# Kernel optimization log

Measured on AMD Instinct MI355X. Metric: run time of the kernel, lower is better.

## Reference

```python
import jax, jax.numpy as jnp
import numpy as np

N, E, IN, ED, H, HID, OUT, G = 50000, 800000, 128, 16, 4, 64, 128, 64
NEG_SLOPE = 0.2


def _glorot(key, shape):
    fan_in, fan_out = shape[0], shape[-1]
    lim = float(np.sqrt(6.0 / (fan_in + fan_out)))
    return jax.random.uniform(key, shape, jnp.float32, -lim, lim)


def setup_inputs() -> dict:
    key = jax.random.key(0)
    ks = jax.random.split(key, 32)
    inp = {}
    inp['x'] = jax.random.normal(ks[0], (N, IN), jnp.float32)
    inp['edge_index'] = jax.random.randint(ks[1], (2, E), 0, N)
    inp['edge_attr'] = jax.random.normal(ks[2], (E, ED), jnp.float32)
    inp['batch'] = jnp.sort(jax.random.randint(ks[3], (N,), 0, G))
    # layer dims: (in_channels, out_channels_per_head, concat)
    dims = [(IN, HID, True), (H * HID, HID, True), (H * HID, OUT, False)]
    k = 4
    for i, (cin, c, concat) in enumerate(dims):
        inp[f'W{i}'] = _glorot(ks[k], (cin, H * c)); k += 1
        inp[f'asrc{i}'] = _glorot(ks[k], (1, H, c)); k += 1
        inp[f'adst{i}'] = _glorot(ks[k], (1, H, c)); k += 1
        inp[f'We{i}'] = _glorot(ks[k], (ED, H * c)); k += 1
        inp[f'ae{i}'] = _glorot(ks[k], (1, H, c)); k += 1
        inp[f'b{i}'] = jnp.zeros((H * c if concat else c,), jnp.float32); k += 1
    return inp


def _gat_layer(x, src, dst, ea, W, asrc, adst, We, ae, b, c, concat):
    # PyG GATConv math (eval mode, shared lin for src/dst, edge_dim set).
    n = x.shape[0]
    h = (x @ W).reshape(n, H, c)                      # [N,H,C]
    a_s = (h * asrc).sum(-1)                          # [N,H]
    a_d = (h * adst).sum(-1)                          # [N,H]
    e = (ea @ We).reshape(-1, H, c)                   # [Etot,H,C]
    a_e = (e * ae).sum(-1)                            # [Etot,H]
    alpha = jax.nn.leaky_relu(a_s[src] + a_d[dst] + a_e, NEG_SLOPE)
    # numerically stable per-destination softmax (every dst has a self-loop)
    amax = jax.ops.segment_max(alpha, dst, num_segments=n)
    ex = jnp.exp(alpha - amax[dst])
    denom = jax.ops.segment_sum(ex, dst, num_segments=n)
    alpha = ex / (denom[dst] + 1e-16)
    out = jax.ops.segment_sum(h[src] * alpha[..., None], dst, num_segments=n)
    out = out.reshape(n, H * c) if concat else out.mean(axis=1)
    return out + b


def reference(x, edge_index, edge_attr, batch,
              W0, asrc0, adst0, We0, ae0, b0,
              W1, asrc1, adst1, We1, ae1, b1,
              W2, asrc2, adst2, We2, ae2, b2):
    n = x.shape[0]
    loop = jnp.arange(n)
    src = jnp.concatenate([edge_index[0], loop])
    dst = jnp.concatenate([edge_index[1], loop])
    # self-loop edge_attr uses fill_value='mean' (PyG default)
    ea = jnp.concatenate(
        [edge_attr, jnp.broadcast_to(edge_attr.mean(0), (n, edge_attr.shape[1]))], axis=0)
    h = _gat_layer(x, src, dst, ea, W0, asrc0, adst0, We0, ae0, b0, HID, True)
    h = jax.nn.elu(h)
    h = _gat_layer(h, src, dst, ea, W1, asrc1, adst1, We1, ae1, b1, HID, True)
    h = jax.nn.elu(h)
    h = _gat_layer(h, src, dst, ea, W2, asrc2, adst2, We2, ae2, b2, OUT, False)
    # global mean pool over graphs
    gsum = jax.ops.segment_sum(h, batch, num_segments=G)
    cnt = jax.ops.segment_sum(jnp.ones((n,), h.dtype), batch, num_segments=G)
    return gsum / jnp.maximum(cnt, 1.0)[:, None]
```

## Files before the change

kernel.cpp:

```cpp
#include <hip/hip_runtime.h>
#include <hip/hip_bf16.h>
#include <hip/hip_fp16.h>
#include <math.h>

#define N_NODES 50000
#define N_EDGES 800000
#define NHEADS  4
#define NEG_SLOPE 0.2f

typedef __attribute__((ext_vector_type(8))) _Float16 half8v;
typedef __attribute__((ext_vector_type(4))) float f32x4;

__device__ __forceinline__ void gld_lds16(const ushort* g, ushort* l) {
  __builtin_amdgcn_global_load_lds(
      (const __attribute__((address_space(1))) void*)g,
      (__attribute__((address_space(3))) void*)l, 16, 0, 0);
}

__device__ __forceinline__ void fma4(float4& a, uint2 r, float e) {
  __half2 p = *(__half2*)&r.x, q = *(__half2*)&r.y;
  float2 f = __half22float2(p), g2 = __half22float2(q);
  a.x += e * f.x; a.y += e * f.y; a.z += e * g2.x; a.w += e * g2.y;
}

__global__ void tofp16_kernel(const float* __restrict__ in, __half* __restrict__ out,
                              int n4) {
  int i = blockIdx.x * blockDim.x + threadIdx.x;
  if (i >= n4) return;
  float4 v = ((const float4*)in)[i];
  __half2 a = __floats2half2_rn(v.x, v.y);
  __half2 b = __floats2half2_rn(v.z, v.w);
  ((__half2*)out)[2 * i] = a;
  ((__half2*)out)[2 * i + 1] = b;
}

__global__ void splitT16_kernel(const float* __restrict__ W, __half* __restrict__ hi,
                                __half* __restrict__ lo, int kshift, int N, int n) {
  int i = blockIdx.x * blockDim.x + threadIdx.x;
  if (i >= n) return;
  int K = 1 << kshift;
  int nn = i >> kshift, k = i & (K - 1);
  float v = W[(size_t)k * N + nn];
  __half h = __float2half(v);
  hi[i] = h;
  lo[i] = __float2half(v - __half2float(h));
}

__global__ __launch_bounds__(256) void gemm_mfma_kernel(
    const __half* __restrict__ Ah, const __half* __restrict__ Bth,
    const __half* __restrict__ Btl, __half* __restrict__ h16,
    const float* __restrict__ asrc, const float* __restrict__ adst,
    float* __restrict__ a_s, float* __restrict__ a_d, int M, int K, int N, int Cph) {
  __shared__ ushort lds[3 * 4096];
  int tid = threadIdx.x;
  int lane = tid & 63, w = tid >> 6;
  int wm = w >> 1, wn = w & 1;
  int r16 = lane & 15, kgrp = lane >> 4;
  int bm = blockIdx.y * 128, bn = blockIdx.x * 128;

  const ushort* gp[6];
#pragma unroll
  for (int i = 0; i < 6; ++i) {
    int c = i * 256 + tid;
    int mmat = c >> 9;
    int s = c & 511;
    int row = s >> 2;
    int kg = (s & 3) ^ ((row >> 1) & 3);
    const ushort* base;
    int rowg;
    if (mmat == 0)      { base = (const ushort*)Ah;  rowg = min(bm + row, M - 1); }
    else if (mmat == 1) { base = (const ushort*)Bth; rowg = bn + row; }
    else                { base = (const ushort*)Btl; rowg = bn + row; }
    gp[i] = base + (size_t)rowg * K + kg * 8;
  }

  f32x4 acc[4][4] = {};
  for (int k0 = 0; k0 < K; k0 += 32) {
#pragma unroll
    for (int i = 0; i < 6; ++i)
      gld_lds16(gp[i] + k0, lds + i * 2048 + tid * 8);
    __syncthreads();
    half8v ah[4], bh[4], bl[4];
#pragma unroll
    for (int m = 0; m < 4; ++m) {
      int row = wm * 64 + m * 16 + r16;
      int s = row * 4 + (kgrp ^ ((row >> 1) & 3));
      ah[m] = *(const half8v*)(lds + 0 * 4096 + s * 8);
    }
#pragma unroll
    for (int j = 0; j < 4; ++j) {
      int row = wn * 64 + j * 16 + r16;
      int s = row * 4 + (kgrp ^ ((row >> 1) & 3));
      bh[j] = *(const half8v*)(lds + 1 * 4096 + s * 8);
      bl[j] = *(const half8v*)(lds + 2 * 4096 + s * 8);
    }
#pragma unroll
    for (int m = 0; m < 4; ++m)
#pragma unroll
      for (int j = 0; j < 4; ++j) {
        acc[m][j] = __builtin_amdgcn_mfma_f32_16x16x32_f16(ah[m], bh[j], acc[m][j], 0, 0, 0);
        acc[m][j] = __builtin_amdgcn_mfma_f32_16x16x32_f16(ah[m], bl[j], acc[m][j], 0, 0, 0);
      }
    __syncthreads();
  }

  int colbase = bn + wn * 64;
  int hd = colbase / Cph;
#pragma unroll
  for (int m = 0; m < 4; ++m) {
#pragma unroll
    for (int r = 0; r < 4; ++r) {
      int row = bm + wm * 64 + m * 16 + kgrp * 4 + r;
      bool ok = row < M;
      float ps = 0.f, pd = 0.f;
#pragma unroll
      for (int j = 0; j < 4; ++j) {
        float val = acc[m][j][r];
        int col = colbase + 16 * j + r16;
        if (ok) h16[(size_t)row * N + col] = __float2half(val);
        ps += val * asrc[col];
        pd += val * adst[col];
      }
#pragma unroll
      for (int o = 8; o >= 1; o >>= 1) {
        ps += __shfl_xor(ps, o);
        pd += __shfl_xor(pd, o);
      }
      if (r16 == 0 && ok) {
        atomicAdd(&a_s[row * NHEADS + hd], ps);
        atomicAdd(&a_d[row * NHEADS + hd], pd);
      }
    }
  }
}

__global__ void ea_colsum_kernel(const float* __restrict__ ea,
                                 float* __restrict__ sums, int E) {
  int tid = threadIdx.x;
  int col = tid & 15;
  float s = 0.f;
  for (int r = blockIdx.x * 16 + (tid >> 4); r < E; r += gridDim.x * 16)
    s += ea[(size_t)r * 16 + col];
  __shared__ float red[256];
  red[tid] = s;
  __syncthreads();
  for (int off = 128; off >= 16; off >>= 1) {
    if (tid < off) red[tid] += red[tid + off];
    __syncthreads();
  }
  if (tid < 16) atomicAdd(&sums[tid], red[tid]);
}

__global__ void wvec_kernel(const float* __restrict__ We0, const float* __restrict__ ae0,
                            const float* __restrict__ We1, const float* __restrict__ ae1,
                            const float* __restrict__ We2, const float* __restrict__ ae2,
                            const float* __restrict__ ea_sum,
                            float* __restrict__ wvec, float* __restrict__ ae_self) {
  __shared__ float sw[192];
  int tid = threadIdx.x;
  if (tid < 192) {
    int l = tid >> 6, rem = tid & 63, k = rem >> 2, hd = rem & 3;
    int C = (l == 2) ? 128 : 64;
    const float* We = (l == 0) ? We0 : (l == 1) ? We1 : We2;
    const float* ae = (l == 0) ? ae0 : (l == 1) ? ae1 : ae2;
    float s = 0.f;
    for (int c = 0; c < C; ++c) s += We[(size_t)k * (4 * C) + hd * C + c] * ae[hd * C + c];
    sw[tid] = s;
    wvec[tid] = s;
  }
  __syncthreads();
  if (tid < 12) {
    int l = tid >> 2, hd = tid & 3;
    const float invE = 1.0f / (float)N_EDGES;
    float s = 0.f;
    for (int k = 0; k < 16; ++k) s += ea_sum[k] * invE * sw[l * 64 + k * 4 + hd];
    ae_self[tid] = s;
  }
}

__global__ void ae_csr_kernel(const float* __restrict__ ea, const float* __restrict__ wv,
                              const float* __restrict__ ae_self,
                              const int* __restrict__ csr_eid,
                              float* __restrict__ aec, int tot, int E) {
  int i = blockIdx.x * blockDim.x + threadIdx.x;
  int stride = gridDim.x * blockDim.x;
  for (int p = i; p < tot; p += stride) {
    int eid = csr_eid[p];
    if (eid >= E) {
#pragma unroll
      for (int l = 0; l < 3; ++l)
        *(float4*)(aec + ((size_t)l * tot + p) * 4) =
            make_float4(ae_self[l * 4 + 0], ae_self[l * 4 + 1],
                        ae_self[l * 4 + 2], ae_self[l * 4 + 3]);
    } else {
      float row[16];
      const float4* rp = (const float4*)(ea + (size_t)eid * 16);
#pragma unroll
      for (int q = 0; q < 4; ++q) {
        float4 v = rp[q];
        row[q * 4 + 0] = v.x; row[q * 4 + 1] = v.y;
        row[q * 4 + 2] = v.z; row[q * 4 + 3] = v.w;
      }
#pragma unroll
      for (int l = 0; l < 3; ++l) {
        float s0 = 0, s1 = 0, s2 = 0, s3 = 0;
#pragma unroll
        for (int k = 0; k < 16; ++k) {
          float v = row[k];
          s0 += v * wv[l * 64 + k * 4 + 0];
          s1 += v * wv[l * 64 + k * 4 + 1];
          s2 += v * wv[l * 64 + k * 4 + 2];
          s3 += v * wv[l * 64 + k * 4 + 3];
        }
        *(float4*)(aec + ((size_t)l * tot + p) * 4) = make_float4(s0, s1, s2, s3);
      }
    }
  }
}

__global__ void deg_init_kernel(int* deg, int n) {
  int i = blockIdx.x * blockDim.x + threadIdx.x;
  if (i < n) deg[i] = 1;
}
__global__ void deg_count_kernel(const int* __restrict__ dst, int* deg, int E) {
  int i = blockIdx.x * blockDim.x + threadIdx.x;
  int s = gridDim.x * blockDim.x;
  for (; i < E; i += s) atomicAdd(&deg[dst[i]], 1);
}
__global__ void scan_kernel(const int* __restrict__ deg, int* __restrict__ offsets,
                            int* __restrict__ cursor, int n) {
  __shared__ int sums[1024];
  int tid = threadIdx.x;
  int chunk = (n + 1023) >> 10;
  int lo = tid * chunk; if (lo > n) lo = n;
  int hi = lo + chunk;  if (hi > n) hi = n;
  int s = 0;
  for (int i = lo; i < hi; ++i) s += deg[i];
  sums[tid] = s;
  __syncthreads();
  for (int d = 1; d < 1024; d <<= 1) {
    int v = (tid >= d) ? sums[tid - d] : 0;
    __syncthreads();
    sums[tid] += v;
    __syncthreads();
  }
  int run = (tid > 0) ? sums[tid - 1] : 0;
  for (int i = lo; i < hi; ++i) {
    offsets[i] = run;
    cursor[i] = run;
    run += deg[i];
  }
  if (tid == 0) offsets[n] = sums[1023];
}
__global__ void scatter_kernel(const int* __restrict__ src, const int* __restrict__ dst,
                               int* cursor, int* __restrict__ csr_src,
                               int* __restrict__ csr_eid, int E, int n) {
  int i = blockIdx.x * blockDim.x + threadIdx.x;
  int s = gridDim.x * blockDim.x;
  int tot = E + n;
  for (; i < tot; i += s) {
    int ss, dd, eid;
    if (i < E) { ss = src[i]; dd = dst[i]; eid = i; }
    else       { ss = i - E; dd = ss;     eid = E; }
    int pos = atomicAdd(&cursor[dd], 1);
    csr_src[pos] = ss;
    csr_eid[pos] = eid;
  }
}

template <int C, int MODE>
__global__ __launch_bounds__(256) void agg_kernel(
    const __half* __restrict__ h, const float* __restrict__ a_s,
    const float* __restrict__ a_d, const float* __restrict__ a_e,
    const int* __restrict__ offsets, const int* __restrict__ csr_src,
    const float* __restrict__ bias, __half* __restrict__ y16,
    float* __restrict__ yf) {
  constexpr int HC = NHEADS * C;
  constexpr int SL = HC / 4;
  constexpr int G = 256 / SL;
  constexpr int HSH = (C == 64) ? 4 : 5;

  __shared__ float exbuf[NHEADS][64];
  __shared__ int sbuf[64];
  __shared__ float dshare[NHEADS];
  __shared__ float4 cbuf4[(C == 64) ? 192 : 128];

  int node = blockIdx.x;
  int tid = threadIdx.x;
  int hd = tid >> 6, l = tid & 63;
  int beg = offsets[node], end = offsets[node + 1];
  int deg = end - beg;

  float a_dn = a_d[node * NHEADS + hd];

  int i = tid & (SL - 1);
  int g = tid / SL;
  int hh = i >> HSH;
  float4 acc = make_float4(0.f, 0.f, 0.f, 0.f);

  auto alpha_of = [&](int j, int& s_out) -> float {
    int s = csr_src[j];
    float aev = a_e[(size_t)j * NHEADS + hd];
    float v = a_s[s * NHEADS + hd] + a_dn + aev;
    s_out = s;
    return (v > 0.f) ? v : NEG_SLOPE * v;
  };

  auto accum_chunk = [&](int cnt) {
    int t = g;
    for (; t + 3 * G < cnt; t += 4 * G) {
      int s0 = sbuf[t], s1 = sbuf[t + G], s2 = sbuf[t + 2 * G], s3 = sbuf[t + 3 * G];
      float e0 = exbuf[hh][t], e1 = exbuf[hh][t + G];
      float e2 = exbuf[hh][t + 2 * G], e3 = exbuf[hh][t + 3 * G];
      uint2 r0 = *(const uint2*)(h + (size_t)s0 * HC + 4 * i);
      uint2 r1 = *(const uint2*)(h + (size_t)s1 * HC + 4 * i);
      uint2 r2 = *(const uint2*)(h + (size_t)s2 * HC + 4 * i);
      uint2 r3 = *(const uint2*)(h + (size_t)s3 * HC + 4 * i);
      fma4(acc, r0, e0); fma4(acc, r1, e1); fma4(acc, r2, e2); fma4(acc, r3, e3);
    }
    for (; t < cnt; t += G) {
      int s0 = sbuf[t];
      float e0 = exbuf[hh][t];
      uint2 r0 = *(const uint2*)(h + (size_t)s0 * HC + 4 * i);
      fma4(acc, r0, e0);
    }
  };

  if (deg <= 64) {
    int j = beg + l;
    bool valid = j < end;
    int s = 0;
    float al = -1e30f;
    if (valid) al = alpha_of(j, s);
    float m = al;
#pragma unroll
    for (int o = 32; o >= 1; o >>= 1) m = fmaxf(m, __shfl_xor(m, o));
    float ex = valid ? __expf(al - m) : 0.f;
    float dsum = ex;
#pragma unroll
    for (int o = 32; o >= 1; o >>= 1) dsum += __shfl_xor(dsum, o);
    exbuf[hd][l] = ex;
    if (hd == 0) sbuf[l] = s;
    if (l == 0) dshare[hd] = dsum;
    __syncthreads();
    accum_chunk(deg);
  } else {
    float m = -1e30f;
    for (int j0 = beg; j0 < end; j0 += 64) {
      int j = j0 + l;
      if (j < end) {
        int s;
        m = fmaxf(m, alpha_of(j, s));
      }
    }
#pragma unroll
    for (int o = 32; o >= 1; o >>= 1) m = fmaxf(m, __shfl_xor(m, o));
    float dsum = 0.f;
    for (int j0 = beg; j0 < end; j0 += 64) {
      int j = j0 + l;
      int cnt = min(64, end - j0);
      float ex = 0.f;
      int s = 0;
      if (j < end) {
        float al = alpha_of(j, s);
        ex = __expf(al - m);
      }
      dsum += ex;
      __syncthreads();
      exbuf[hd][l] = ex;
      if (hd == 0) sbuf[l] = s;
      __syncthreads();
      accum_chunk(cnt);
    }
#pragma unroll
    for (int o = 32; o >= 1; o >>= 1) dsum += __shfl_xor(dsum, o);
    if (l == 0) dshare[hd] = dsum;
    __syncthreads();
  }

  if (MODE == 0) {
    if (g > 0) cbuf4[(g - 1) * SL + i] = acc;
    __syncthreads();
    if (g == 0) {
      float4 c1 = cbuf4[i], c2 = cbuf4[SL + i], c3 = cbuf4[2 * SL + i];
      acc.x += c1.x + c2.x + c3.x;
      acc.y += c1.y + c2.y + c3.y;
      acc.z += c1.z + c2.z + c3.z;
      acc.w += c1.w + c2.w + c3.w;
      float inv = 1.f / (dshare[hh] + 1e-16f);
      const float4 bv = *(const float4*)(bias + 4 * i);
      float o0 = acc.x * inv + bv.x, o1 = acc.y * inv + bv.y;
      float o2 = acc.z * inv + bv.z, o3 = acc.w * inv + bv.w;
      o0 = (o0 > 0.f) ? o0 : (__expf(o0) - 1.f);
      o1 = (o1 > 0.f) ? o1 : (__expf(o1) - 1.f);
      o2 = (o2 > 0.f) ? o2 : (__expf(o2) - 1.f);
      o3 = (o3 > 0.f) ? o3 : (__expf(o3) - 1.f);
      __half2 w0 = __floats2half2_rn(o0, o1);
      __half2 w1 = __floats2half2_rn(o2, o3);
      uint2 pk;
      pk.x = *(uint*)&w0;
      pk.y = *(uint*)&w1;
      *(uint2*)(y16 + (size_t)node * HC + 4 * i) = pk;
    }
  } else {
    if (g == 1) cbuf4[i] = acc;
    __syncthreads();
    if (g == 0) {
      float4 c1 = cbuf4[i];
      float inv = 1.f / (dshare[hh] + 1e-16f);
      acc.x = (acc.x + c1.x) * inv;
      acc.y = (acc.y + c1.y) * inv;
      acc.z = (acc.z + c1.z) * inv;
      acc.w = (acc.w + c1.w) * inv;
    }
    __syncthreads();
    if (g == 0) cbuf4[i] = acc;
    __syncthreads();
    if (tid < 32) {
      float4 s0 = cbuf4[tid], s1 = cbuf4[tid + 32];
      float4 s2 = cbuf4[tid + 64], s3 = cbuf4[tid + 96];
      const float4 bv = *(const float4*)(bias + 4 * tid);
      float4 o;
      o.x = (s0.x + s1.x + s2.x + s3.x) * 0.25f + bv.x;
      o.y = (s0.y + s1.y + s2.y + s3.y) * 0.25f + bv.y;
      o.z = (s0.z + s1.z + s2.z + s3.z) * 0.25f + bv.z;
      o.w = (s0.w + s1.w + s2.w + s3.w) * 0.25f + bv.w;
      *(float4*)(yf + (size_t)node * 128 + 4 * tid) = o;
    }
  }
}

__global__ void pool_kernel(const float* __restrict__ y, const int* __restrict__ batch,
                            float* __restrict__ pool, float* __restrict__ cnt, int n) {
  int n0 = blockIdx.x * 256;
  if (n0 >= n) return;
  int n1 = min(n0 + 256, n);
  int c = threadIdx.x;
  float accum = 0.f;
  int cur = batch[n0];
  int cn = 0;
  for (int nd = n0; nd < n1; ++nd) {
    int g = batch[nd];
    if (g != cur) {
      atomicAdd(&pool[cur * 128 + c], accum);
      if (c == 0) atomicAdd(&cnt[cur], (float)cn);
      accum = 0.f; cn = 0; cur = g;
    }
    accum += y[(size_t)nd * 128 + c];
    cn++;
  }
  atomicAdd(&pool[cur * 128 + c], accum);
  if (c == 0) atomicAdd(&cnt[cur], (float)cn);
}
__global__ void finalize_kernel(const float* __restrict__ pool,
                                const float* __restrict__ cnt, float* __restrict__ out) {
  int i = blockIdx.x * blockDim.x + threadIdx.x;
  if (i < 64 * 128) out[i] = pool[i] / fmaxf(cnt[i >> 7], 1.f);
}

extern "C" void kernel_launch(void* const* d_in, const int* in_sizes, int n_in,
                              void* d_out, int out_size, void* d_ws, size_t ws_size,
                              hipStream_t stream) {
  const float* x = (const float*)d_in[0];
  const int* ei = (const int*)d_in[1];
  const float* ea = (const float*)d_in[2];
  const int* batch = (const int*)d_in[3];
  const float* W[3]    = {(const float*)d_in[4],  (const float*)d_in[10], (const float*)d_in[16]};
  const float* asrc[3] = {(const float*)d_in[5],  (const float*)d_in[11], (const float*)d_in[17]};
  const float* adst[3] = {(const float*)d_in[6],  (const float*)d_in[12], (const float*)d_in[18]};
  const float* Wep[3]  = {(const float*)d_in[7],  (const float*)d_in[13], (const float*)d_in[19]};
  const float* aep[3]  = {(const float*)d_in[8],  (const float*)d_in[14], (const float*)d_in[20]};
  const float* bp[3]   = {(const float*)d_in[9],  (const float*)d_in[15], (const float*)d_in[21]};

  char* ws = (char*)d_ws;
  size_t off = 0;
  auto take = [&](size_t bytes) -> void* {
    void* p = ws + off;
    off = (off + bytes + 255) & ~(size_t)255;
    return p;
  };
  const int TOT = N_EDGES + N_NODES;
  float* zero_region = (float*)take((16 + 8192 + 64) * 4);
  float* ea_sum = zero_region;
  float* pool   = zero_region + 16;
  float* cnt    = zero_region + 16 + 8192;
  float* wvec    = (float*)take(192 * 4);
  float* ae_self = (float*)take(12 * 4);
  int* deg     = (int*)take((size_t)N_NODES * 4);
  int* offsets = (int*)take(((size_t)N_NODES + 1) * 4);
  int* cursor  = (int*)take((size_t)N_NODES * 4);
  int* csr_src = (int*)take((size_t)TOT * 4);
  int* csr_eid = (int*)take((size_t)TOT * 4);
  float* a_s  = (float*)take((size_t)N_NODES * NHEADS * 4);
  float* a_d  = (float*)take((size_t)N_NODES * NHEADS * 4);
  float* aec  = (float*)take((size_t)3 * TOT * NHEADS * 4);
  __half* x16 = (__half*)take((size_t)N_NODES * 128 * 2);
  __half* Bth = (__half*)take((size_t)512 * 256 * 2);
  __half* Btl = (__half*)take((size_t)512 * 256 * 2);
  __half* h16 = (__half*)take((size_t)N_NODES * 512 * 2);
  __half* y16 = (__half*)take((size_t)N_NODES * 256 * 2);
  float* ybuf = (float*)take((size_t)N_NODES * 128 * 4);

  const int* srcp = ei;
  const int* dstp = ei + N_EDGES;

  hipMemsetAsync(zero_region, 0, (16 + 8192 + 64) * 4, stream);
  ea_colsum_kernel<<<512, 256, 0, stream>>>(ea, ea_sum, N_EDGES);
  deg_init_kernel<<<(N_NODES + 255) / 256, 256, 0, stream>>>(deg, N_NODES);
  deg_count_kernel<<<2048, 256, 0, stream>>>(dstp, deg, N_EDGES);
  scan_kernel<<<1, 1024, 0, stream>>>(deg, offsets, cursor, N_NODES);
  scatter_kernel<<<2048, 256, 0, stream>>>(srcp, dstp, cursor, csr_src, csr_eid,
                                           N_EDGES, N_NODES);
  wvec_kernel<<<1, 256, 0, stream>>>(Wep[0], aep[0], Wep[1], aep[1], Wep[2], aep[2],
                                     ea_sum, wvec, ae_self);
  ae_csr_kernel<<<2048, 256, 0, stream>>>(ea, wvec, ae_self, csr_eid, aec, TOT, N_EDGES);
  tofp16_kernel<<<(N_NODES * 128 / 4 + 255) / 256, 256, 0, stream>>>(x, x16,
                                                                     N_NODES * 128 / 4);

  const __half* Acur = x16;
  for (int l = 0; l < 3; ++l) {
    int K = (l == 0) ? 128 : 256;
    int kshift = (l == 0) ? 7 : 8;
    int C = (l == 2) ? 128 : 64;
    int HC = NHEADS * C;
    hipMemsetAsync(a_s, 0, (size_t)N_NODES * NHEADS * 4 * 2, stream);
    int nB = HC * K;
    splitT16_kernel<<<(nB + 255) / 256, 256, 0, stream>>>(W[l], Bth, Btl, kshift, HC, nB);
    gemm_mfma_kernel<<<dim3(HC / 128, (N_NODES + 127) / 128), 256, 0, stream>>>(
        Acur, Bth, Btl, h16, asrc[l], adst[l], a_s, a_d, N_NODES, K, HC, C);
    if (l < 2) {
      agg_kernel<64, 0><<<N_NODES, 256, 0, stream>>>(
          h16, a_s, a_d, aec + (size_t)l * TOT * NHEADS, offsets, csr_src, bp[l],
          y16, nullptr);
      Acur = y16;
    } else {
      agg_kernel<128, 1><<<N_NODES, 256, 0, stream>>>(
          h16, a_s, a_d, aec + (size_t)l * TOT * NHEADS, offsets, csr_src, bp[l],
          nullptr, ybuf);
    }
  }
  pool_kernel<<<(N_NODES + 255) / 256, 128, 0, stream>>>(ybuf, batch, pool, cnt, N_NODES);
  finalize_kernel<<<(8192 + 255) / 256, 256, 0, stream>>>(pool, cnt, (float*)d_out);
}
```

Before: 817.4 us.

## Parallelize CSR scan, merge weight splits and memsets, pack CSR src/eid

Swaps the single-block serial degree scan for a three-kernel parallel block scan, and folds the +1 self-loop count into that scan so the degree-init kernel is no longer needed. The three per-layer weight transpose/split launches become one kernel before the layer loop, and the per-layer a_s/a_d memsets become a single up-front memset over a contiguous zero region. Scatter writes a packed (src,eid) pair, which ae_csr_kernel unpacks into csr_src. The goal is to remove the serial scan bottleneck and several small launches, in exchange for more workspace and extra passes over the packed array.

```diff
diff --git a/kernel.cpp b/kernel.cpp
--- a/kernel.cpp
+++ b/kernel.cpp
@@ -34,16 +34,27 @@
   ((__half2*)out)[2 * i + 1] = b;
 }
 
-__global__ void splitT16_kernel(const float* __restrict__ W, __half* __restrict__ hi,
-                                __half* __restrict__ lo, int kshift, int N, int n) {
-  int i = blockIdx.x * blockDim.x + threadIdx.x;
-  if (i >= n) return;
+__global__ void splitT_all_kernel(const float* __restrict__ W0,
+                                  const float* __restrict__ W1,
+                                  const float* __restrict__ W2,
+                                  __half* __restrict__ B0h, __half* __restrict__ B0l,
+                                  __half* __restrict__ B1h, __half* __restrict__ B1l,
+                                  __half* __restrict__ B2h, __half* __restrict__ B2l) {
+  int i = blockIdx.x * 256 + threadIdx.x;
+  if (i >= 229376) return;
+  const float* W;
+  __half *bh, *bl;
+  int kshift, N, base;
+  if (i < 32768)       { W = W0; bh = B0h; bl = B0l; kshift = 7; N = 256; base = 0; }
+  else if (i < 98304)  { W = W1; bh = B1h; bl = B1l; kshift = 8; N = 256; base = 32768; }
+  else                 { W = W2; bh = B2h; bl = B2l; kshift = 8; N = 512; base = 98304; }
+  int j = i - base;
   int K = 1 << kshift;
-  int nn = i >> kshift, k = i & (K - 1);
+  int nn = j >> kshift, k = j & (K - 1);
   float v = W[(size_t)k * N + nn];
   __half h = __float2half(v);
-  hi[i] = h;
-  lo[i] = __float2half(v - __half2float(h));
+  bh[j] = h;
+  bl[j] = __float2half(v - __half2float(h));
 }
 
 __global__ __launch_bounds__(256) void gemm_mfma_kernel(
@@ -178,14 +189,78 @@
   }
 }
 
+__global__ void deg_count_kernel(const int* __restrict__ dst, int* deg, int E) {
+  int i = blockIdx.x * blockDim.x + threadIdx.x;
+  int s = gridDim.x * blockDim.x;
+  for (; i < E; i += s) atomicAdd(&deg[dst[i]], 1);
+}
+
+__global__ void scan_a_kernel(const int* __restrict__ deg, int* __restrict__ tmp,
+                              int* __restrict__ bsum, int n) {
+  __shared__ int s[256];
+  int i = blockIdx.x * 256 + threadIdx.x;
+  int v = (i < n) ? (deg[i] + 1) : 0;
+  s[threadIdx.x] = v;
+  __syncthreads();
+  for (int d = 1; d < 256; d <<= 1) {
+    int t = (threadIdx.x >= d) ? s[threadIdx.x - d] : 0;
+    __syncthreads();
+    s[threadIdx.x] += t;
+    __syncthreads();
+  }
+  if (i < n) tmp[i] = s[threadIdx.x] - v;
+  if (threadIdx.x == 255) bsum[blockIdx.x] = s[255];
+}
+__global__ void scan_b_kernel(int* bsum, int nb) {
+  __shared__ int s[256];
+  int v = (threadIdx.x < nb) ? bsum[threadIdx.x] : 0;
+  s[threadIdx.x] = v;
+  __syncthreads();
+  for (int d = 1; d < 256; d <<= 1) {
+    int t = (threadIdx.x >= d) ? s[threadIdx.x - d] : 0;
+    __syncthreads();
+    s[threadIdx.x] += t;
+    __syncthreads();
+  }
+  if (threadIdx.x < nb) bsum[threadIdx.x] = s[threadIdx.x] - v;
+}
+__global__ void scan_c_kernel(const int* __restrict__ tmp, const int* __restrict__ bsum,
+                              int* __restrict__ offsets, int* __restrict__ cursor,
+                              int n, int tot) {
+  int i = blockIdx.x * 256 + threadIdx.x;
+  if (i < n) {
+    int o = tmp[i] + bsum[blockIdx.x];
+    offsets[i] = o;
+    cursor[i] = o;
+  }
+  if (i == 0) offsets[n] = tot;
+}
+
+__global__ void scatter_kernel(const int* __restrict__ src, const int* __restrict__ dst,
+                               int* cursor, uint2* __restrict__ csr_pack, int E, int n) {
+  int i = blockIdx.x * blockDim.x + threadIdx.x;
+  int s = gridDim.x * blockDim.x;
+  int tot = E + n;
+  for (; i < tot; i += s) {
+    int ss, dd, eid;
+    if (i < E) { ss = src[i]; dd = dst[i]; eid = i; }
+    else       { ss = i - E; dd = ss;     eid = E; }
+    int pos = atomicAdd(&cursor[dd], 1);
+    csr_pack[pos] = make_uint2((uint)ss, (uint)eid);
+  }
+}
+
 __global__ void ae_csr_kernel(const float* __restrict__ ea, const float* __restrict__ wv,
                               const float* __restrict__ ae_self,
-                              const int* __restrict__ csr_eid,
-                              float* __restrict__ aec, int tot, int E) {
+                              const uint2* __restrict__ csr_pack,
+                              float* __restrict__ aec, int* __restrict__ csr_src,
+                              int tot, int E) {
   int i = blockIdx.x * blockDim.x + threadIdx.x;
   int stride = gridDim.x * blockDim.x;
   for (int p = i; p < tot; p += stride) {
-    int eid = csr_eid[p];
+    uint2 pk = csr_pack[p];
+    int eid = (int)pk.y;
+    csr_src[p] = (int)pk.x;
     if (eid >= E) {
 #pragma unroll
       for (int l = 0; l < 3; ++l)
@@ -215,56 +290,6 @@
         *(float4*)(aec + ((size_t)l * tot + p) * 4) = make_float4(s0, s1, s2, s3);
       }
     }
-  }
-}
-
-__global__ void deg_init_kernel(int* deg, int n) {
-  int i = blockIdx.x * blockDim.x + threadIdx.x;
-  if (i < n) deg[i] = 1;
-}
-__global__ void deg_count_kernel(const int* __restrict__ dst, int* deg, int E) {
-  int i = blockIdx.x * blockDim.x + threadIdx.x;
-  int s = gridDim.x * blockDim.x;
-  for (; i < E; i += s) atomicAdd(&deg[dst[i]], 1);
-}
-__global__ void scan_kernel(const int* __restrict__ deg, int* __restrict__ offsets,
-                            int* __restrict__ cursor, int n) {
-  __shared__ int sums[1024];
-  int tid = threadIdx.x;
-  int chunk = (n + 1023) >> 10;
-  int lo = tid * chunk; if (lo > n) lo = n;
-  int hi = lo + chunk;  if (hi > n) hi = n;
-  int s = 0;
-  for (int i = lo; i < hi; ++i) s += deg[i];
-  sums[tid] = s;
-  __syncthreads();
-  for (int d = 1; d < 1024; d <<= 1) {
-    int v = (tid >= d) ? sums[tid - d] : 0;
-    __syncthreads();
-    sums[tid] += v;
-    __syncthreads();
-  }
-  int run = (tid > 0) ? sums[tid - 1] : 0;
-  for (int i = lo; i < hi; ++i) {
-    offsets[i] = run;
-    cursor[i] = run;
-    run += deg[i];
-  }
-  if (tid == 0) offsets[n] = sums[1023];
-}
-__global__ void scatter_kernel(const int* __restrict__ src, const int* __restrict__ dst,
-                               int* cursor, int* __restrict__ csr_src,
-                               int* __restrict__ csr_eid, int E, int n) {
-  int i = blockIdx.x * blockDim.x + threadIdx.x;
-  int s = gridDim.x * blockDim.x;
-  int tot = E + n;
-  for (; i < tot; i += s) {
-    int ss, dd, eid;
-    if (i < E) { ss = src[i]; dd = dst[i]; eid = i; }
-    else       { ss = i - E; dd = ss;     eid = E; }
-    int pos = atomicAdd(&cursor[dd], 1);
-    csr_src[pos] = ss;
-    csr_eid[pos] = eid;
   }
 }
 
@@ -480,54 +505,61 @@
     return p;
   };
   const int TOT = N_EDGES + N_NODES;
-  float* zero_region = (float*)take((16 + 8192 + 64) * 4);
-  float* ea_sum = zero_region;
-  float* pool   = zero_region + 16;
-  float* cnt    = zero_region + 16 + 8192;
+  size_t zero_begin = off;
+  float* ea_sum = (float*)take(16 * 4);
+  float* pool   = (float*)take(8192 * 4);
+  float* cnt    = (float*)take(64 * 4);
+  int*   deg    = (int*)take((size_t)N_NODES * 4);
+  float* a_sd   = (float*)take((size_t)3 * 2 * N_NODES * NHEADS * 4);
+  size_t zero_bytes = off - zero_begin;
+
   float* wvec    = (float*)take(192 * 4);
   float* ae_self = (float*)take(12 * 4);
-  int* deg     = (int*)take((size_t)N_NODES * 4);
+  int* tmp     = (int*)take((size_t)N_NODES * 4);
+  int* bsum    = (int*)take(256 * 4);
   int* offsets = (int*)take(((size_t)N_NODES + 1) * 4);
   int* cursor  = (int*)take((size_t)N_NODES * 4);
+  uint2* csr_pack = (uint2*)take((size_t)TOT * 8);
   int* csr_src = (int*)take((size_t)TOT * 4);
-  int* csr_eid = (int*)take((size_t)TOT * 4);
-  float* a_s  = (float*)take((size_t)N_NODES * NHEADS * 4);
-  float* a_d  = (float*)take((size_t)N_NODES * NHEADS * 4);
   float* aec  = (float*)take((size_t)3 * TOT * NHEADS * 4);
   __half* x16 = (__half*)take((size_t)N_NODES * 128 * 2);
-  __half* Bth = (__half*)take((size_t)512 * 256 * 2);
-  __half* Btl = (__half*)take((size_t)512 * 256 * 2);
+  __half* Bh[3], *Bl[3];
+  Bh[0] = (__half*)take((size_t)32768 * 2);  Bl[0] = (__half*)take((size_t)32768 * 2);
+  Bh[1] = (__half*)take((size_t)65536 * 2);  Bl[1] = (__half*)take((size_t)65536 * 2);
+  Bh[2] = (__half*)take((size_t)131072 * 2); Bl[2] = (__half*)take((size_t)131072 * 2);
   __half* h16 = (__half*)take((size_t)N_NODES * 512 * 2);
   __half* y16 = (__half*)take((size_t)N_NODES * 256 * 2);
   float* ybuf = (float*)take((size_t)N_NODES * 128 * 4);
 
   const int* srcp = ei;
   const int* dstp = ei + N_EDGES;
-
-  hipMemsetAsync(zero_region, 0, (16 + 8192 + 64) * 4, stream);
+  const int NB = (N_NODES + 255) / 256;
+
+  hipMemsetAsync(ws + zero_begin, 0, zero_bytes, stream);
   ea_colsum_kernel<<<512, 256, 0, stream>>>(ea, ea_sum, N_EDGES);
-  deg_init_kernel<<<(N_NODES + 255) / 256, 256, 0, stream>>>(deg, N_NODES);
   deg_count_kernel<<<2048, 256, 0, stream>>>(dstp, deg, N_EDGES);
-  scan_kernel<<<1, 1024, 0, stream>>>(deg, offsets, cursor, N_NODES);
-  scatter_kernel<<<2048, 256, 0, stream>>>(srcp, dstp, cursor, csr_src, csr_eid,
-                                           N_EDGES, N_NODES);
+  scan_a_kernel<<<NB, 256, 0, stream>>>(deg, tmp, bsum, N_NODES);
+  scan_b_kernel<<<1, 256, 0, stream>>>(bsum, NB);
+  scan_c_kernel<<<NB, 256, 0, stream>>>(tmp, bsum, offsets, cursor, N_NODES, TOT);
+  scatter_kernel<<<2048, 256, 0, stream>>>(srcp, dstp, cursor, csr_pack, N_EDGES, N_NODES);
   wvec_kernel<<<1, 256, 0, stream>>>(Wep[0], aep[0], Wep[1], aep[1], Wep[2], aep[2],
                                      ea_sum, wvec, ae_self);
-  ae_csr_kernel<<<2048, 256, 0, stream>>>(ea, wvec, ae_self, csr_eid, aec, TOT, N_EDGES);
+  ae_csr_kernel<<<2048, 256, 0, stream>>>(ea, wvec, ae_self, csr_pack, aec, csr_src,
+                                          TOT, N_EDGES);
   tofp16_kernel<<<(N_NODES * 128 / 4 + 255) / 256, 256, 0, stream>>>(x, x16,
                                                                      N_NODES * 128 / 4);
+  splitT_all_kernel<<<(229376 + 255) / 256, 256, 0, stream>>>(
+      W[0], W[1], W[2], Bh[0], Bl[0], Bh[1], Bl[1], Bh[2], Bl[2]);
 
   const __half* Acur = x16;
   for (int l = 0; l < 3; ++l) {
     int K = (l == 0) ? 128 : 256;
-    int kshift = (l == 0) ? 7 : 8;
     int C = (l == 2) ? 128 : 64;
     int HC = NHEADS * C;
-    hipMemsetAsync(a_s, 0, (size_t)N_NODES * NHEADS * 4 * 2, stream);
-    int nB = HC * K;
-    splitT16_kernel<<<(nB + 255) / 256, 256, 0, stream>>>(W[l], Bth, Btl, kshift, HC, nB);
+    float* a_s = a_sd + (size_t)l * 2 * N_NODES * NHEADS;
+    float* a_d = a_s + (size_t)N_NODES * NHEADS;
     gemm_mfma_kernel<<<dim3(HC / 128, (N_NODES + 127) / 128), 256, 0, stream>>>(
-        Acur, Bth, Btl, h16, asrc[l], adst[l], a_s, a_d, N_NODES, K, HC, C);
+        Acur, Bh[l], Bl[l], h16, asrc[l], adst[l], a_s, a_d, N_NODES, K, HC, C);
     if (l < 2) {
       agg_kernel<64, 0><<<N_NODES, 256, 0, stream>>>(
           h16, a_s, a_d, aec + (size_t)l * TOT * NHEADS, offsets, csr_src, bp[l],
@@ -539,6 +571,6 @@
           nullptr, ybuf);
     }
   }
-  pool_kernel<<<(N_NODES + 255) / 256, 128, 0, stream>>>(ybuf, batch, pool, cnt, N_NODES);
+  pool_kernel<<<NB, 128, 0, stream>>>(ybuf, batch, pool, cnt, N_NODES);
   finalize_kernel<<<(8192 + 255) / 256, 256, 0, stream>>>(pool, cnt, (float*)d_out);
 }
```

Measured after the change: 719.1 us. 1.14x faster.
